# Performance work log

Hardware: AMD Instinct MI355X
Metric: run time of the kernel (lower is better)

## Reference

```python
import jax, jax.numpy as jnp
import numpy as np

B, C, P, H, W, K = 8, 64, 64, 256, 256, 3
BN_EPS = 1e-5


def setup_inputs() -> dict:
    key = jax.random.key(0)
    k0, k1, k2, k3 = jax.random.split(key, 4)
    x = jax.random.normal(k0, (B, C, H, W), dtype=jnp.float32)
    dw_w = jax.random.normal(k1, (C, K, K), dtype=jnp.float32) * (1.0 / K)
    pw_w = jax.random.normal(k2, (P, C), dtype=jnp.float32) * (1.0 / np.sqrt(C))
    gamma = jnp.ones((P,), dtype=jnp.float32)
    beta = jnp.zeros((P,), dtype=jnp.float32)
    mean = jnp.zeros((P,), dtype=jnp.float32)
    var = jnp.ones((P,), dtype=jnp.float32)
    conv_w = jax.random.normal(k3, (1, P), dtype=jnp.float32) * (1.0 / np.sqrt(P))
    return dict(x=x, dw_w=dw_w, pw_w=pw_w, gamma=gamma, beta=beta,
                mean=mean, var=var, conv_w=conv_w)


def reference(x, dw_w, pw_w, gamma, beta, mean, var, conv_w):
    # Faithful to the torch forward: x[:, i:] = relu6(dw_conv[i](x[:, i:i+1]))
    # broadcasts each 1-channel result over channels i..C-1, so iteration i
    # consumes iteration i-1's output -> a sequential chain seeded by x[:, 0].
    def step(y, w):  # y: [B, H, W], w: [K, K]
        o = jax.lax.conv_general_dilated(
            y[:, None, :, :], w[None, None, :, :],
            window_strides=(1, 1), padding='SAME')[:, 0]
        o = jnp.clip(o, 0.0, 6.0)  # ReLU6
        return o, o

    _, ys = jax.lax.scan(step, x[:, 0], dw_w)      # [C, B, H, W]

    # pointwise conv (1x1, no bias)
    h = jnp.einsum('pc,cbhw->bphw', pw_w, ys)       # [B, P, H, W]

    # BatchNorm (inference form with running stats) + ReLU6
    scale = gamma * jax.lax.rsqrt(var + BN_EPS)
    h = h * scale[None, :, None, None] + (beta - mean * scale)[None, :, None, None]
    h = jnp.clip(h, 0.0, 6.0)

    # final 1x1 conv P -> 1 (no bias)
    out = jnp.einsum('op,bphw->bohw', conv_w, h)    # [B, 1, H, W]
    return out
```

## Files before the change

### kernel.cpp

```cpp
#include <hip/hip_runtime.h>
#include <hip/hip_bf16.h>

#define B_    8
#define C_    64
#define P_    64
#define H_    256
#define W_    256
#define BHW_  (B_ * H_ * W_)
#define BN_EPS 1e-5f

#define CHUNK 16
#define SWC   64

__device__ __forceinline__ float dpp_row_shr1(float v) {
    return __int_as_float(__builtin_amdgcn_update_dpp(
        0, __float_as_int(v), 0x111, 0xF, 0xF, true));
}
__device__ __forceinline__ float dpp_row_shl1(float v) {
    return __int_as_float(__builtin_amdgcn_update_dpp(
        0, __float_as_int(v), 0x101, 0xF, 0xF, true));
}

__global__ __launch_bounds__(1024, 8) void chain_kernel(
    const float* __restrict__ src,
    size_t src_batch_stride,
    const float* __restrict__ dw,
    float* __restrict__ ys,
    int c0)
{
    __shared__ __align__(16) float buf0[66 * SWC];
    __shared__ __align__(16) float buf1[66 * SWC];

    const int tid = threadIdx.x;
    const int row = tid >> 4;
    const int seg = tid & 15;
    const int lx  = seg * 4;
    const int b   = blockIdx.z;
    const int ty0 = blockIdx.y * 32;
    const int tx0 = blockIdx.x * 32;
    const int gy  = ty0 - 16 + row;
    const int gx  = tx0 - 16 + lx;
    const bool inImg = (gy >= 0) && (gy < H_) && (gx >= 0) && (gx < W_);
    const float msk = inImg ? 1.0f : 0.0f;

    float4 v = make_float4(0.f, 0.f, 0.f, 0.f);
    if (inImg)
        v = *(const float4*)(src + (size_t)b * src_batch_stride
                             + (size_t)gy * W_ + gx);

    float* cur = buf0;
    float* nxt = buf1;
    const int cell = (row + 1) * SWC + lx;
    *(float4*)&cur[cell] = v;
    if (row == 0) {
        float4 z = make_float4(0.f, 0.f, 0.f, 0.f);
        *(float4*)&buf0[lx] = z;  *(float4*)&buf0[65 * SWC + lx] = z;
        *(float4*)&buf1[lx] = z;  *(float4*)&buf1[65 * SWC + lx] = z;
    }
    __syncthreads();

    const bool wOK = (row >= 16) && (row < 48) && (seg >= 4) && (seg < 12);
    float* gbase = ys + (size_t)c0 * BHW_ + ((size_t)b * H_ + gy) * W_ + gx;

#pragma unroll
    for (int i = 0; i < CHUNK; ++i) {
        const float w0 = dw[i*9+0], w1 = dw[i*9+1], w2 = dw[i*9+2];
        const float w3 = dw[i*9+3], w4 = dw[i*9+4], w5 = dw[i*9+5];
        const float w6 = dw[i*9+6], w7 = dw[i*9+7], w8 = dw[i*9+8];

        float4 rT = *(const float4*)&cur[cell - SWC];
        float4 rM = *(const float4*)&cur[cell];
        float4 rB = *(const float4*)&cur[cell + SWC];

        float tl = dpp_row_shr1(rT.w), tr = dpp_row_shl1(rT.x);
        float ml = dpp_row_shr1(rM.w), mr = dpp_row_shl1(rM.x);
        float bl = dpp_row_shr1(rB.w), br = dpp_row_shl1(rB.x);

        float4 ov;
        {
            float s0 = fmaf(tl,   w0, fmaf(rT.x, w1, fmaf(rT.y, w2,
                       fmaf(ml,   w3, fmaf(rM.x, w4, fmaf(rM.y, w5,
                       fmaf(bl,   w6, fmaf(rB.x, w7, rB.y * w8))))))));
            float s1 = fmaf(rT.x, w0, fmaf(rT.y, w1, fmaf(rT.z, w2,
                       fmaf(rM.x, w3, fmaf(rM.y, w4, fmaf(rM.z, w5,
                       fmaf(rB.x, w6, fmaf(rB.y, w7, rB.z * w8))))))));
            float s2 = fmaf(rT.y, w0, fmaf(rT.z, w1, fmaf(rT.w, w2,
                       fmaf(rM.y, w3, fmaf(rM.z, w4, fmaf(rM.w, w5,
                       fmaf(rB.y, w6, fmaf(rB.z, w7, rB.w * w8))))))));
            float s3 = fmaf(rT.z, w0, fmaf(rT.w, w1, fmaf(tr,   w2,
                       fmaf(rM.z, w3, fmaf(rM.w, w4, fmaf(mr,   w5,
                       fmaf(rB.z, w6, fmaf(rB.w, w7, br   * w8))))))));
            ov.x = fminf(fmaxf(s0, 0.f), 6.f) * msk;
            ov.y = fminf(fmaxf(s1, 0.f), 6.f) * msk;
            ov.z = fminf(fmaxf(s2, 0.f), 6.f) * msk;
            ov.w = fminf(fmaxf(s3, 0.f), 6.f) * msk;
        }

        if (i < CHUNK - 1) {
            *(float4*)&nxt[cell] = ov;
            __syncthreads();
            float* tmp = cur; cur = nxt; nxt = tmp;
        }
        if (wOK)
            *(float4*)(gbase + (size_t)i * BHW_) = ov;
    }
}

__global__ __launch_bounds__(256) void fuse_kernel(
    const float* __restrict__ ys,
    const float* __restrict__ pw_w,
    const float* __restrict__ gamma,
    const float* __restrict__ beta,
    const float* __restrict__ mean,
    const float* __restrict__ var,
    const float* __restrict__ conv_w,
    float* __restrict__ out)
{
    __shared__ float As[C_ * P_];
    __shared__ float bias_s[P_];
    __shared__ float cw_s[P_];

    const int tid = threadIdx.x;

    for (int idx = tid; idx < C_ * P_; idx += 256) {
        int p = idx & 63;
        int c = idx >> 6;
        float scale = gamma[p] / sqrtf(var[p] + BN_EPS);
        As[idx] = pw_w[p * C_ + c] * scale;
    }
    if (tid < P_) {
        float scale = gamma[tid] / sqrtf(var[tid] + BN_EPS);
        bias_s[tid] = beta[tid] - mean[tid] * scale;
        cw_s[tid]   = conv_w[tid];
    }
    __syncthreads();

    const size_t n0 = (size_t)blockIdx.x * 512 + tid;
    const size_t n1 = n0 + 256;

    float h0[P_], h1[P_];
#pragma unroll
    for (int p = 0; p < P_; ++p) { h0[p] = 0.f; h1[p] = 0.f; }

#pragma unroll 2
    for (int c = 0; c < C_; ++c) {
        float y0 = ys[(size_t)c * BHW_ + n0];
        float y1 = ys[(size_t)c * BHW_ + n1];
        const float* arow = &As[c * P_];
#pragma unroll
        for (int p = 0; p < P_; ++p) {
            float av = arow[p];
            h0[p] = fmaf(av, y0, h0[p]);
            h1[p] = fmaf(av, y1, h1[p]);
        }
    }

    float acc0 = 0.f, acc1 = 0.f;
#pragma unroll
    for (int p = 0; p < P_; ++p) {
        float v0 = fminf(fmaxf(h0[p] + bias_s[p], 0.f), 6.f);
        float v1 = fminf(fmaxf(h1[p] + bias_s[p], 0.f), 6.f);
        acc0 = fmaf(cw_s[p], v0, acc0);
        acc1 = fmaf(cw_s[p], v1, acc1);
    }
    out[n0] = acc0;
    out[n1] = acc1;
}

extern "C" void kernel_launch(void* const* d_in, const int* in_sizes, int n_in,
                              void* d_out, int out_size, void* d_ws, size_t ws_size,
                              hipStream_t stream) {
    const float* x      = (const float*)d_in[0];
    const float* dw_w   = (const float*)d_in[1];
    const float* pw_w   = (const float*)d_in[2];
    const float* gamma  = (const float*)d_in[3];
    const float* beta   = (const float*)d_in[4];
    const float* mean   = (const float*)d_in[5];
    const float* var    = (const float*)d_in[6];
    const float* conv_w = (const float*)d_in[7];
    float* out = (float*)d_out;

    float* ys = (float*)d_ws;

    dim3 cgrid(W_ / 32, H_ / 32, B_);

    chain_kernel<<<cgrid, 1024, 0, stream>>>(
        x, (size_t)C_ * H_ * W_, dw_w, ys, 0);

    for (int k = 1; k < C_ / CHUNK; ++k) {
        int c0 = k * CHUNK;
        chain_kernel<<<cgrid, 1024, 0, stream>>>(
            ys + (size_t)(c0 - 1) * BHW_, (size_t)H_ * W_,
            dw_w + c0 * 9, ys, c0);
    }

    fuse_kernel<<<BHW_ / 512, 256, 0, stream>>>(
        ys, pw_w, gamma, beta, mean, var, conv_w, out);
}
```

Baseline: 294.6 us.

## Merge chain launches into one cooperative kernel with grid sync; precompute fused weights

The four per-chunk chain kernel launches become a single cooperative launch that loops over chunks and uses grid.sync between them. One block also precomputes the BN-scaled pointwise weights, bias and final conv weights into workspace. A new fuse kernel (one pixel per thread, weights read from global) uses them when the workspace is large enough, otherwise the old fuse kernel runs. This removes launch gaps and the per-block weight setup, at the cost of grid-wide barrier overhead and the requirement that all 512 blocks of 1024 threads be co-resident.

```diff
diff --git a/kernel.cpp b/kernel.cpp
--- a/kernel.cpp
+++ b/kernel.cpp
@@ -1,5 +1,8 @@
 #include <hip/hip_runtime.h>
 #include <hip/hip_bf16.h>
+#include <hip/hip_cooperative_groups.h>
+
+namespace cg = cooperative_groups;
 
 #define B_    8
 #define C_    64
@@ -21,13 +24,21 @@
         0, __float_as_int(v), 0x101, 0xF, 0xF, true));
 }
 
-__global__ __launch_bounds__(1024, 8) void chain_kernel(
-    const float* __restrict__ src,
-    size_t src_batch_stride,
-    const float* __restrict__ dw,
+__global__ __launch_bounds__(1024, 8) void chain_coop(
+    const float* __restrict__ x,
+    const float* __restrict__ dw_w,
     float* __restrict__ ys,
-    int c0)
+    const float* __restrict__ pw_w,
+    const float* __restrict__ gamma,
+    const float* __restrict__ beta,
+    const float* __restrict__ mean,
+    const float* __restrict__ var,
+    const float* __restrict__ conv_w,
+    float* __restrict__ prep_out,
+    int do_prep)
 {
+    cg::grid_group grid = cg::this_grid();
+
     __shared__ __align__(16) float buf0[66 * SWC];
     __shared__ __align__(16) float buf1[66 * SWC];
 
@@ -42,42 +53,59 @@
     const int gx  = tx0 - 16 + lx;
     const bool inImg = (gy >= 0) && (gy < H_) && (gx >= 0) && (gx < W_);
     const float msk = inImg ? 1.0f : 0.0f;
-
-    float4 v = make_float4(0.f, 0.f, 0.f, 0.f);
-    if (inImg)
-        v = *(const float4*)(src + (size_t)b * src_batch_stride
-                             + (size_t)gy * W_ + gx);
-
-    float* cur = buf0;
-    float* nxt = buf1;
     const int cell = (row + 1) * SWC + lx;
-    *(float4*)&cur[cell] = v;
+    const bool wOK = (row >= 16) && (row < 48) && (seg >= 4) && (seg < 12);
+    const long long goff = (long long)(b * H_ + gy) * W_ + gx;
+
+    if (do_prep && blockIdx.x == 0 && blockIdx.y == 0 && blockIdx.z == 0) {
+        for (int idx = tid; idx < C_ * P_; idx += 1024) {
+            int p = idx & 63;
+            int c = idx >> 6;
+            float sc = gamma[p] / sqrtf(var[p] + BN_EPS);
+            prep_out[idx] = pw_w[p * C_ + c] * sc;
+        }
+        if (tid < P_) {
+            float sc = gamma[tid] / sqrtf(var[tid] + BN_EPS);
+            prep_out[4096 + tid] = beta[tid] - mean[tid] * sc;
+            prep_out[4160 + tid] = conv_w[tid];
+        }
+    }
+
     if (row == 0) {
         float4 z = make_float4(0.f, 0.f, 0.f, 0.f);
         *(float4*)&buf0[lx] = z;  *(float4*)&buf0[65 * SWC + lx] = z;
         *(float4*)&buf1[lx] = z;  *(float4*)&buf1[65 * SWC + lx] = z;
     }
-    __syncthreads();
-
-    const bool wOK = (row >= 16) && (row < 48) && (seg >= 4) && (seg < 12);
-    float* gbase = ys + (size_t)c0 * BHW_ + ((size_t)b * H_ + gy) * W_ + gx;
-
-#pragma unroll
-    for (int i = 0; i < CHUNK; ++i) {
-        const float w0 = dw[i*9+0], w1 = dw[i*9+1], w2 = dw[i*9+2];
-        const float w3 = dw[i*9+3], w4 = dw[i*9+4], w5 = dw[i*9+5];
-        const float w6 = dw[i*9+6], w7 = dw[i*9+7], w8 = dw[i*9+8];
-
-        float4 rT = *(const float4*)&cur[cell - SWC];
-        float4 rM = *(const float4*)&cur[cell];
-        float4 rB = *(const float4*)&cur[cell + SWC];
-
-        float tl = dpp_row_shr1(rT.w), tr = dpp_row_shl1(rT.x);
-        float ml = dpp_row_shr1(rM.w), mr = dpp_row_shl1(rM.x);
-        float bl = dpp_row_shr1(rB.w), br = dpp_row_shl1(rB.x);
-
-        float4 ov;
-        {
+
+    for (int k = 0; k < C_ / CHUNK; ++k) {
+        const float* in = (k == 0)
+            ? x + (size_t)b * (C_ * H_ * W_)
+            : ys + (size_t)(CHUNK * k - 1) * BHW_ + (size_t)b * (H_ * W_);
+        float4 v = make_float4(0.f, 0.f, 0.f, 0.f);
+        if (inImg)
+            v = *(const float4*)(in + (size_t)gy * W_ + gx);
+
+        float* cur = buf0;
+        float* nxt = buf1;
+        *(float4*)&cur[cell] = v;
+        __syncthreads();
+
+        const float* dwk = dw_w + k * (CHUNK * 9);
+
+#pragma unroll
+        for (int i = 0; i < CHUNK; ++i) {
+            const float w0 = dwk[i*9+0], w1 = dwk[i*9+1], w2 = dwk[i*9+2];
+            const float w3 = dwk[i*9+3], w4 = dwk[i*9+4], w5 = dwk[i*9+5];
+            const float w6 = dwk[i*9+6], w7 = dwk[i*9+7], w8 = dwk[i*9+8];
+
+            float4 rT = *(const float4*)&cur[cell - SWC];
+            float4 rM = *(const float4*)&cur[cell];
+            float4 rB = *(const float4*)&cur[cell + SWC];
+
+            float tl = dpp_row_shr1(rT.w), tr = dpp_row_shl1(rT.x);
+            float ml = dpp_row_shr1(rM.w), mr = dpp_row_shl1(rM.x);
+            float bl = dpp_row_shr1(rB.w), br = dpp_row_shl1(rB.x);
+
             float s0 = fmaf(tl,   w0, fmaf(rT.x, w1, fmaf(rT.y, w2,
                        fmaf(ml,   w3, fmaf(rM.x, w4, fmaf(rM.y, w5,
                        fmaf(bl,   w6, fmaf(rB.x, w7, rB.y * w8))))))));
@@ -90,20 +118,57 @@
             float s3 = fmaf(rT.z, w0, fmaf(rT.w, w1, fmaf(tr,   w2,
                        fmaf(rM.z, w3, fmaf(rM.w, w4, fmaf(mr,   w5,
                        fmaf(rB.z, w6, fmaf(rB.w, w7, br   * w8))))))));
+            float4 ov;
             ov.x = fminf(fmaxf(s0, 0.f), 6.f) * msk;
             ov.y = fminf(fmaxf(s1, 0.f), 6.f) * msk;
             ov.z = fminf(fmaxf(s2, 0.f), 6.f) * msk;
             ov.w = fminf(fmaxf(s3, 0.f), 6.f) * msk;
-        }
-
-        if (i < CHUNK - 1) {
-            *(float4*)&nxt[cell] = ov;
-            __syncthreads();
-            float* tmp = cur; cur = nxt; nxt = tmp;
-        }
-        if (wOK)
-            *(float4*)(gbase + (size_t)i * BHW_) = ov;
-    }
+
+            if (i < CHUNK - 1) {
+                *(float4*)&nxt[cell] = ov;
+                __syncthreads();
+                float* tmp = cur; cur = nxt; nxt = tmp;
+            }
+            if (wOK)
+                *(float4*)(ys + (size_t)(CHUNK * k + i) * BHW_ + goff) = ov;
+        }
+
+        if (k < C_ / CHUNK - 1) {
+            __threadfence();
+            grid.sync();
+        }
+    }
+}
+
+__global__ __launch_bounds__(256) void fuse2(
+    const float* __restrict__ ys,
+    const float* __restrict__ prep,
+    float* __restrict__ out)
+{
+    const size_t n = (size_t)blockIdx.x * 256 + threadIdx.x;
+
+    float h[P_];
+#pragma unroll
+    for (int p = 0; p < P_; ++p) h[p] = 0.f;
+
+#pragma unroll 4
+    for (int c = 0; c < C_; ++c) {
+        float y = ys[(size_t)c * BHW_ + n];
+        const float* a = prep + c * P_;
+#pragma unroll
+        for (int p = 0; p < P_; ++p)
+            h[p] = fmaf(a[p], y, h[p]);
+    }
+
+    const float* bias = prep + 4096;
+    const float* cw   = prep + 4160;
+    float acc = 0.f;
+#pragma unroll
+    for (int p = 0; p < P_; ++p) {
+        float v = fminf(fmaxf(h[p] + bias[p], 0.f), 6.f);
+        acc = fmaf(cw[p], v, acc);
+    }
+    out[n] = acc;
 }
 
 __global__ __launch_bounds__(256) void fuse_kernel(
@@ -121,7 +186,6 @@
     __shared__ float cw_s[P_];
 
     const int tid = threadIdx.x;
-
     for (int idx = tid; idx < C_ * P_; idx += 256) {
         int p = idx & 63;
         int c = idx >> 6;
@@ -137,11 +201,9 @@
 
     const size_t n0 = (size_t)blockIdx.x * 512 + tid;
     const size_t n1 = n0 + 256;
-
     float h0[P_], h1[P_];
 #pragma unroll
     for (int p = 0; p < P_; ++p) { h0[p] = 0.f; h1[p] = 0.f; }
-
 #pragma unroll 2
     for (int c = 0; c < C_; ++c) {
         float y0 = ys[(size_t)c * BHW_ + n0];
@@ -154,7 +216,6 @@
             h1[p] = fmaf(av, y1, h1[p]);
         }
     }
-
     float acc0 = 0.f, acc1 = 0.f;
 #pragma unroll
     for (int p = 0; p < P_; ++p) {
@@ -181,19 +242,22 @@
     float* out = (float*)d_out;
 
     float* ys = (float*)d_ws;
-
-    dim3 cgrid(W_ / 32, H_ / 32, B_);
-
-    chain_kernel<<<cgrid, 1024, 0, stream>>>(
-        x, (size_t)C_ * H_ * W_, dw_w, ys, 0);
-
-    for (int k = 1; k < C_ / CHUNK; ++k) {
-        int c0 = k * CHUNK;
-        chain_kernel<<<cgrid, 1024, 0, stream>>>(
-            ys + (size_t)(c0 - 1) * BHW_, (size_t)H_ * W_,
-            dw_w + c0 * 9, ys, c0);
-    }
-
-    fuse_kernel<<<BHW_ / 512, 256, 0, stream>>>(
-        ys, pw_w, gamma, beta, mean, var, conv_w, out);
-}
+    const size_t ys_bytes = (size_t)C_ * BHW_ * sizeof(float);
+    const bool big = ws_size >= ys_bytes + 17 * 1024;
+    float* prep = (float*)((char*)d_ws + ys_bytes);
+    int do_prep = big ? 1 : 0;
+
+    void* kargs[] = {
+        (void*)&x, (void*)&dw_w, (void*)&ys, (void*)&pw_w, (void*)&gamma,
+        (void*)&beta, (void*)&mean, (void*)&var, (void*)&conv_w,
+        (void*)&prep, (void*)&do_prep
+    };
+    hipLaunchCooperativeKernel(chain_coop, dim3(8, 8, 8), dim3(1024, 1, 1),
+                               kargs, 0u, stream);
+
+    if (big)
+        fuse2<<<BHW_ / 256, 256, 0, stream>>>(ys, prep, out);
+    else
+        fuse_kernel<<<BHW_ / 512, 256, 0, stream>>>(
+            ys, pw_w, gamma, beta, mean, var, conv_w, out);
+}
```

After: 872.6 us. +196.2%, slower.

## Use split-bf16 MFMA for pointwise conv in fused epilogue kernel

Applied to the files above, without the earlier changes.

Replaces the scalar-FMA pointwise 64x64 matmul with bf16 MFMA instructions. Both weights and activations are split into high and low bf16 parts, and three MFMAs per tile pair approximate fp32 accuracy. Activations are staged through padded LDS in bf16 and the kernel becomes a grid-stride loop over 64-pixel tiles with 1024 blocks. The goal is to remove the VALU-bound FMA cost and the heavy register use of the old kernel, at the cost of extra conversion work, LDS traffic and a small loss of precision.

```diff
diff --git a/kernel.cpp b/kernel.cpp
--- a/kernel.cpp
+++ b/kernel.cpp
@@ -20,6 +20,18 @@
     return __int_as_float(__builtin_amdgcn_update_dpp(
         0, __float_as_int(v), 0x101, 0xF, 0xF, true));
 }
+
+__device__ __forceinline__ short f2bf(float x) {
+    unsigned u = __float_as_uint(x);
+    unsigned r = (u + 0x7FFFu + ((u >> 16) & 1u)) >> 16;
+    return (short)r;
+}
+__device__ __forceinline__ float bf2f(short h) {
+    return __uint_as_float(((unsigned)(unsigned short)h) << 16);
+}
+
+typedef __attribute__((ext_vector_type(8))) short bf16x8;
+typedef __attribute__((ext_vector_type(4))) float f32x4;
 
 __global__ __launch_bounds__(1024, 8) void chain_kernel(
     const float* __restrict__ src,
@@ -76,25 +88,23 @@
         float ml = dpp_row_shr1(rM.w), mr = dpp_row_shl1(rM.x);
         float bl = dpp_row_shr1(rB.w), br = dpp_row_shl1(rB.x);
 
+        float s0 = fmaf(tl,   w0, fmaf(rT.x, w1, fmaf(rT.y, w2,
+                   fmaf(ml,   w3, fmaf(rM.x, w4, fmaf(rM.y, w5,
+                   fmaf(bl,   w6, fmaf(rB.x, w7, rB.y * w8))))))));
+        float s1 = fmaf(rT.x, w0, fmaf(rT.y, w1, fmaf(rT.z, w2,
+                   fmaf(rM.x, w3, fmaf(rM.y, w4, fmaf(rM.z, w5,
+                   fmaf(rB.x, w6, fmaf(rB.y, w7, rB.z * w8))))))));
+        float s2 = fmaf(rT.y, w0, fmaf(rT.z, w1, fmaf(rT.w, w2,
+                   fmaf(rM.y, w3, fmaf(rM.z, w4, fmaf(rM.w, w5,
+                   fmaf(rB.y, w6, fmaf(rB.z, w7, rB.w * w8))))))));
+        float s3 = fmaf(rT.z, w0, fmaf(rT.w, w1, fmaf(tr,   w2,
+                   fmaf(rM.z, w3, fmaf(rM.w, w4, fmaf(mr,   w5,
+                   fmaf(rB.z, w6, fmaf(rB.w, w7, br   * w8))))))));
         float4 ov;
-        {
-            float s0 = fmaf(tl,   w0, fmaf(rT.x, w1, fmaf(rT.y, w2,
-                       fmaf(ml,   w3, fmaf(rM.x, w4, fmaf(rM.y, w5,
-                       fmaf(bl,   w6, fmaf(rB.x, w7, rB.y * w8))))))));
-            float s1 = fmaf(rT.x, w0, fmaf(rT.y, w1, fmaf(rT.z, w2,
-                       fmaf(rM.x, w3, fmaf(rM.y, w4, fmaf(rM.z, w5,
-                       fmaf(rB.x, w6, fmaf(rB.y, w7, rB.z * w8))))))));
-            float s2 = fmaf(rT.y, w0, fmaf(rT.z, w1, fmaf(rT.w, w2,
-                       fmaf(rM.y, w3, fmaf(rM.z, w4, fmaf(rM.w, w5,
-                       fmaf(rB.y, w6, fmaf(rB.z, w7, rB.w * w8))))))));
-            float s3 = fmaf(rT.z, w0, fmaf(rT.w, w1, fmaf(tr,   w2,
-                       fmaf(rM.z, w3, fmaf(rM.w, w4, fmaf(mr,   w5,
-                       fmaf(rB.z, w6, fmaf(rB.w, w7, br   * w8))))))));
-            ov.x = fminf(fmaxf(s0, 0.f), 6.f) * msk;
-            ov.y = fminf(fmaxf(s1, 0.f), 6.f) * msk;
-            ov.z = fminf(fmaxf(s2, 0.f), 6.f) * msk;
-            ov.w = fminf(fmaxf(s3, 0.f), 6.f) * msk;
-        }
+        ov.x = fminf(fmaxf(s0, 0.f), 6.f) * msk;
+        ov.y = fminf(fmaxf(s1, 0.f), 6.f) * msk;
+        ov.z = fminf(fmaxf(s2, 0.f), 6.f) * msk;
+        ov.w = fminf(fmaxf(s3, 0.f), 6.f) * msk;
 
         if (i < CHUNK - 1) {
             *(float4*)&nxt[cell] = ov;
@@ -106,7 +116,7 @@
     }
 }
 
-__global__ __launch_bounds__(256) void fuse_kernel(
+__global__ __launch_bounds__(256) void fuse_mfma(
     const float* __restrict__ ys,
     const float* __restrict__ pw_w,
     const float* __restrict__ gamma,
@@ -116,55 +126,106 @@
     const float* __restrict__ conv_w,
     float* __restrict__ out)
 {
-    __shared__ float As[C_ * P_];
-    __shared__ float bias_s[P_];
-    __shared__ float cw_s[P_];
-
-    const int tid = threadIdx.x;
-
-    for (int idx = tid; idx < C_ * P_; idx += 256) {
-        int p = idx & 63;
-        int c = idx >> 6;
-        float scale = gamma[p] / sqrtf(var[p] + BN_EPS);
-        As[idx] = pw_w[p * C_ + c] * scale;
-    }
+    __shared__ short yh[64 * 88];
+    __shared__ short yl[64 * 88];
+    __shared__ float2 bc[P_];
+
+    const int tid  = threadIdx.x;
+    const int lane = tid & 63;
+    const int wv   = tid >> 6;
+    const int nIdx = lane & 15;
+    const int quad = lane >> 4;
+
     if (tid < P_) {
-        float scale = gamma[tid] / sqrtf(var[tid] + BN_EPS);
-        bias_s[tid] = beta[tid] - mean[tid] * scale;
-        cw_s[tid]   = conv_w[tid];
+        float sc = gamma[tid] * rsqrtf(var[tid] + BN_EPS);
+        bc[tid] = make_float2(beta[tid] - mean[tid] * sc, conv_w[tid]);
+    }
+
+    bf16x8 Ah[4][2], Al[4][2];
+#pragma unroll
+    for (int pt = 0; pt < 4; ++pt) {
+        const int p = pt * 16 + nIdx;
+        const float sc = gamma[p] * rsqrtf(var[p] + BN_EPS);
+#pragma unroll
+        for (int kt = 0; kt < 2; ++kt) {
+            const float* ap = pw_w + p * C_ + kt * 32 + quad * 8;
+            bf16x8 hh, ll;
+#pragma unroll
+            for (int j = 0; j < 8; ++j) {
+                float a = ap[j] * sc;
+                short h = f2bf(a);
+                hh[j] = h;
+                ll[j] = f2bf(a - bf2f(h));
+            }
+            Ah[pt][kt] = hh;
+            Al[pt][kt] = ll;
+        }
     }
     __syncthreads();
 
-    const size_t n0 = (size_t)blockIdx.x * 512 + tid;
-    const size_t n1 = n0 + 256;
-
-    float h0[P_], h1[P_];
-#pragma unroll
-    for (int p = 0; p < P_; ++p) { h0[p] = 0.f; h1[p] = 0.f; }
-
-#pragma unroll 2
-    for (int c = 0; c < C_; ++c) {
-        float y0 = ys[(size_t)c * BHW_ + n0];
-        float y1 = ys[(size_t)c * BHW_ + n1];
-        const float* arow = &As[c * P_];
-#pragma unroll
-        for (int p = 0; p < P_; ++p) {
-            float av = arow[p];
-            h0[p] = fmaf(av, y0, h0[p]);
-            h1[p] = fmaf(av, y1, h1[p]);
-        }
-    }
-
-    float acc0 = 0.f, acc1 = 0.f;
-#pragma unroll
-    for (int p = 0; p < P_; ++p) {
-        float v0 = fminf(fmaxf(h0[p] + bias_s[p], 0.f), 6.f);
-        float v1 = fminf(fmaxf(h1[p] + bias_s[p], 0.f), 6.f);
-        acc0 = fmaf(cw_s[p], v0, acc0);
-        acc1 = fmaf(cw_s[p], v1, acc1);
-    }
-    out[n0] = acc0;
-    out[n1] = acc1;
+    const int px_ = tid & 63;
+    const int c0_ = (tid >> 6) * 16;
+
+    for (int tile = blockIdx.x; tile < BHW_ / 64; tile += gridDim.x) {
+        const size_t base = (size_t)tile * 64;
+
+        float yv[16];
+#pragma unroll
+        for (int j = 0; j < 16; ++j)
+            yv[j] = ys[(size_t)(c0_ + j) * BHW_ + base + px_];
+
+        __syncthreads();
+
+        short hs[16], ls[16];
+#pragma unroll
+        for (int j = 0; j < 16; ++j) {
+            short h = f2bf(yv[j]);
+            hs[j] = h;
+            ls[j] = f2bf(yv[j] - bf2f(h));
+        }
+        *(bf16x8*)&yh[px_ * 88 + c0_]     = *(bf16x8*)&hs[0];
+        *(bf16x8*)&yh[px_ * 88 + c0_ + 8] = *(bf16x8*)&hs[8];
+        *(bf16x8*)&yl[px_ * 88 + c0_]     = *(bf16x8*)&ls[0];
+        *(bf16x8*)&yl[px_ * 88 + c0_ + 8] = *(bf16x8*)&ls[8];
+
+        __syncthreads();
+
+        f32x4 acc[4];
+#pragma unroll
+        for (int pt = 0; pt < 4; ++pt) acc[pt] = (f32x4){0.f, 0.f, 0.f, 0.f};
+
+        const int col = wv * 16 + nIdx;
+#pragma unroll
+        for (int kt = 0; kt < 2; ++kt) {
+            bf16x8 Bh = *(bf16x8*)&yh[col * 88 + kt * 32 + quad * 8];
+            bf16x8 Bl = *(bf16x8*)&yl[col * 88 + kt * 32 + quad * 8];
+#pragma unroll
+            for (int pt = 0; pt < 4; ++pt) {
+                acc[pt] = __builtin_amdgcn_mfma_f32_16x16x32_bf16(
+                    Ah[pt][kt], Bh, acc[pt], 0, 0, 0);
+                acc[pt] = __builtin_amdgcn_mfma_f32_16x16x32_bf16(
+                    Ah[pt][kt], Bl, acc[pt], 0, 0, 0);
+                acc[pt] = __builtin_amdgcn_mfma_f32_16x16x32_bf16(
+                    Al[pt][kt], Bh, acc[pt], 0, 0, 0);
+            }
+        }
+
+        float sum = 0.f;
+#pragma unroll
+        for (int pt = 0; pt < 4; ++pt) {
+#pragma unroll
+            for (int r = 0; r < 4; ++r) {
+                const int p = pt * 16 + quad * 4 + r;
+                float2 b = bc[p];
+                float v = fminf(fmaxf(acc[pt][r] + b.x, 0.f), 6.f);
+                sum = fmaf(b.y, v, sum);
+            }
+        }
+        sum += __shfl_xor(sum, 16, 64);
+        sum += __shfl_xor(sum, 32, 64);
+        if (lane < 16)
+            out[base + wv * 16 + lane] = sum;
+    }
 }
 
 extern "C" void kernel_launch(void* const* d_in, const int* in_sizes, int n_in,
@@ -186,7 +247,6 @@
 
     chain_kernel<<<cgrid, 1024, 0, stream>>>(
         x, (size_t)C_ * H_ * W_, dw_w, ys, 0);
-
     for (int k = 1; k < C_ / CHUNK; ++k) {
         int c0 = k * CHUNK;
         chain_kernel<<<cgrid, 1024, 0, stream>>>(
@@ -194,6 +254,6 @@
             dw_w + c0 * 9, ys, c0);
     }
 
-    fuse_kernel<<<BHW_ / 512, 256, 0, stream>>>(
+    fuse_mfma<<<1024, 256, 0, stream>>>(
         ys, pw_w, gamma, beta, mean, var, conv_w, out);
 }
```

After: 273.8 us. -7.1%, faster.
